# Kernel tuning notes

Measured on AMD Instinct MI355X. Metric: run time of the kernel, lower is better.

The kernel has to match this reference:

```python
import jax, jax.numpy as jnp
import numpy as np

T, K, B, D, ND = 200, 512, 1024, 128, 16
H = D * ND
LOGC = float(np.log(np.sqrt(2.0 * np.pi)))  # log(sqrt(2*pi))


def setup_inputs() -> dict:
    key = jax.random.key(0)
    ks = jax.random.split(key, 16)
    s = 0.02  # xavier-ish init scale
    X = jax.random.normal(ks[0], (T, K, D), jnp.float32)
    M = (jax.random.uniform(ks[1], (T, K, D)) < 0.7).astype(jnp.float32)
    # K unique, sorted sample indices per time step (ragged chunks made uniform)
    batch_idx = jnp.sort(jnp.argsort(jax.random.uniform(ks[2], (T, B)), axis=1)[:, :K], axis=1).astype(jnp.int32)
    obs_times = jnp.arange(1, T + 1, dtype=jnp.float32) * 0.05
    def mat(k, sh):
        return jax.random.normal(k, sh, jnp.float32) * s
    return {
        'obs_times': obs_times, 'X': X, 'M': M,
        'Wp1': mat(ks[3], (H, H)), 'bp1': jnp.zeros((H,), jnp.float32),
        'Wp2': mat(ks[4], (H, 2 * D)), 'bp2': jnp.zeros((2 * D,), jnp.float32),
        'W_r': mat(ks[5], (D, H)), 'V_r': mat(ks[6], (D, H)), 'U_r': mat(ks[7], (H, H)),
        'W_z': mat(ks[8], (D, H)), 'V_z': mat(ks[9], (D, H)), 'U_z': mat(ks[10], (H, H)),
        'W_h': mat(ks[11], (D, H)), 'V_h': mat(ks[12], (D, H)), 'U_h': mat(ks[13], (H, H)),
        'b_r': jnp.zeros((H,), jnp.float32), 'b_z': jnp.zeros((H,), jnp.float32), 'b_h': jnp.zeros((H,), jnp.float32),
        'Wgx': mat(ks[14], (D, D)), 'Wgh': mat(ks[15], (D, H)),
        'batch_idx': batch_idx, 'num_samples': B,
    }


def _forward(obs_times, X, M, Wp1, bp1, Wp2, bp2, W_r, V_r, U_r, W_z, V_z, U_z,
             W_h, V_h, U_h, b_r, b_z, b_h, Wgx, Wgh, batch_idx, num_samples):
    Bn, Dn, Hn = num_samples, W_r.shape[0], W_r.shape[1]
    h0 = jnp.zeros((Bn, Hn), jnp.float32)
    lx0 = jnp.zeros((Bn, Dn), jnp.float32)
    lt0 = jnp.zeros((Bn, Dn), jnp.float32)

    def step(carry, xs):
        h, last_x, last_t, loss, totM = carry
        t, Xo, Mo, idx = xs
        hg = h[idx]  # [K,H] gather of persistent state for observed samples
        # p_model (dropout in eval mode = identity), only observed rows are used
        p = jnp.maximum(hg @ Wp1 + bp1, 0.0) @ Wp2 + bp2  # [K,2D]
        mean, logvar = jnp.split(p, 2, axis=1)
        err = (Xo - mean) * jnp.exp(-0.5 * logvar)
        losses = 0.5 * ((err * err + logvar + 2.0 * LOGC) * Mo)
        # masked last-observation update (scatter)
        lx = last_x[idx] * (1.0 - Mo) + Xo * Mo
        last_x = last_x.at[idx].set(lx)
        mean_x = jnp.sum(Xo, 0, keepdims=True) / jnp.sum(Mo + 1e-6, 0, keepdims=True)
        ltg = last_t[idx]
        iv = t - ltg  # interval uses pre-update last_t (gathered rows only)
        last_t = last_t.at[idx].set(ltg * (1.0 - Mo) + t * Mo)
        gx = jnp.exp(-jnp.maximum(0.0, iv @ Wgx))  # [K,D]
        gh = jnp.exp(-jnp.maximum(0.0, iv @ Wgh))  # [K,H]
        X_hat = Mo * Xo + (1.0 - Mo) * gx * lx + (1.0 - Mo) * (1.0 - gx) * mean_x
        # GRU-D cell on gathered rows, then scatter back
        hd = gh * hg
        r = jax.nn.sigmoid(X_hat @ W_r + hd @ U_r + Mo @ V_r + b_r)
        z = jax.nn.sigmoid(X_hat @ W_z + hd @ U_z + Mo @ V_z + b_z)
        ht = jnp.tanh(X_hat @ W_h + (r * hd) @ U_h + Mo @ V_h + b_h)
        hn = (1.0 - z) * hd + z * ht
        h = h.at[idx].set(hn)
        return (h, last_x, last_t, loss + losses.sum(), totM + Mo.sum()), None

    init = (h0, lx0, lt0, jnp.float32(0.0), jnp.float32(0.0))
    (h, _, _, loss, totM), _ = jax.lax.scan(step, init, (obs_times, X, M, batch_idx))
    return loss / totM


def reference(obs_times, X, M, Wp1, bp1, Wp2, bp2, W_r, V_r, U_r, W_z, V_z, U_z,
              W_h, V_h, U_h, b_r, b_z, b_h, Wgx, Wgh, batch_idx, num_samples):
    return _forward(obs_times, X, M, Wp1, bp1, Wp2, bp2, W_r, V_r, U_r, W_z, V_z,
                    U_z, W_h, V_h, U_h, b_r, b_z, b_h, Wgx, Wgh, batch_idx, num_samples)
```

## Files before the change

kernel.cpp:

```cpp
#include <hip/hip_runtime.h>

#define TT 200
#define KK 512
#define BB 1024
#define DD 128
#define HH 2048

typedef short short8 __attribute__((ext_vector_type(8)));
typedef float f32x4 __attribute__((ext_vector_type(4)));
typedef __bf16 bf16x8 __attribute__((ext_vector_type(8)));

#define TWO_LOGC 1.8378770664093453f

__device__ __forceinline__ unsigned short f2bf(float f) {
  union { float f; unsigned u; } x; x.f = f;
  unsigned r = x.u + 0x7fffu + ((x.u >> 16) & 1u);
  return (unsigned short)(r >> 16);
}
__device__ __forceinline__ float bf2f(unsigned short b) {
  union { unsigned u; float f; } x; x.u = ((unsigned)b) << 16;
  return x.f;
}
__device__ __forceinline__ f32x4 mfma16(short8 a, short8 b, f32x4 c) {
  return __builtin_amdgcn_mfma_f32_16x16x32_bf16(
      __builtin_bit_cast(bf16x8, a), __builtin_bit_cast(bf16x8, b), c, 0, 0, 0);
}

typedef void __attribute__((address_space(1))) as1_void;
typedef void __attribute__((address_space(3))) as3_void;
__device__ __forceinline__ void gld_lds16(const unsigned short* g, unsigned short* l) {
  __builtin_amdgcn_global_load_lds((as1_void*)const_cast<unsigned short*>(g),
                                   (as3_void*)l, 16, 0, 0);
}

struct GP {
  const unsigned short* A1; int lda1;
  const unsigned short* A2; int lda2; int split;
  const unsigned short* BT; int ldb;
  int Kr;
  const float* bias;
  const float* bias2;
  unsigned short* obf;
  unsigned short* obf2;
  float* of1;
  const float* f1;
  const float* f2;
  const float* f3;
  const unsigned short* u1;
  const int* idx;
  float* h;
  float* d_loss;
};

template <int MI, int NI, int EPI>
__global__ __launch_bounds__(256, 2) void gemmP(GP p) {
  constexpr int BM = 32 * MI, BN = 32 * NI;
  constexpr int L = (MI + NI) / 2;
  __shared__ unsigned short As[4][BM * 32];
  __shared__ unsigned short Bs[4][BN * 32];
  const int tid = threadIdx.x;
  const int lane = tid & 63;
  const int w = tid >> 6;
  const int wr = w >> 1, wc = w & 1;
  const long m0 = (long)blockIdx.x * BM;
  const int n0 = blockIdx.y * BN;

  const int lrow = lane >> 2;
  const unsigned short* gA1[L];
  const unsigned short* gA2[L];
  const unsigned short* gB[L];
  unsigned short* lds0[L];
  int sstr[L];
  bool isA[L];
#pragma unroll
  for (int j = 0; j < L; ++j) {
    int c = w * L + j;
    if (c < 2 * MI) {
      int r = c * 16 + lrow;
      int cs = (lane & 3) ^ ((r >> 1) & 3);
      isA[j] = true;
      gA1[j] = p.A1 + (m0 + r) * (long)p.lda1 + cs * 8;
      gA2[j] = p.A2 + (m0 + r) * (long)p.lda2 + cs * 8 - p.split;
      gB[j] = gA1[j];
      lds0[j] = &As[0][c * 512];
      sstr[j] = BM * 32;
    } else {
      int cb = c - 2 * MI;
      int r = cb * 16 + lrow;
      int cs = (lane & 3) ^ ((r >> 1) & 3);
      isA[j] = false;
      gB[j] = p.BT + (long)(n0 + r) * p.ldb + cs * 8;
      gA1[j] = gB[j]; gA2[j] = gB[j];
      lds0[j] = &Bs[0][cb * 512];
      sstr[j] = BN * 32;
    }
  }

  auto stage = [&](int slot, int k0) {
#pragma unroll
    for (int j = 0; j < L; ++j) {
      const unsigned short* g =
          isA[j] ? ((k0 < p.split) ? gA1[j] + k0 : gA2[j] + k0) : gB[j] + k0;
      gld_lds16(g, lds0[j] + slot * sstr[j]);
    }
  };

  const int frow = lane & 15;
  const int fg = lane >> 4;

  f32x4 acc[MI][NI] = {};

  const int nIter = p.Kr >> 5;
  stage(0, 0);
  stage(1, 32);
  stage(2, 64);
  for (int i = 0; i < nIter; ++i) {
    asm volatile("s_waitcnt vmcnt(%0)" ::"i"(2 * L) : "memory");
    __builtin_amdgcn_s_barrier();
    __builtin_amdgcn_sched_barrier(0);
    const int slot = i & 3;
    short8 af[MI], bfr[NI];
#pragma unroll
    for (int mi = 0; mi < MI; ++mi) {
      int r = wr * (16 * MI) + mi * 16 + frow;
      af[mi] = *(const short8*)&As[slot][r * 32 + ((fg ^ ((r >> 1) & 3)) << 3)];
    }
#pragma unroll
    for (int ni = 0; ni < NI; ++ni) {
      int r = wc * (16 * NI) + ni * 16 + frow;
      bfr[ni] = *(const short8*)&Bs[slot][r * 32 + ((fg ^ ((r >> 1) & 3)) << 3)];
    }
#pragma unroll
    for (int mi = 0; mi < MI; ++mi)
#pragma unroll
      for (int ni = 0; ni < NI; ++ni) acc[mi][ni] = mfma16(af[mi], bfr[ni], acc[mi][ni]);
    int j3 = i + 3;
    if (j3 >= nIter) j3 = nIter - 1;
    stage((i + 3) & 3, j3 * 32);
  }

  float lsum = 0.f;
#pragma unroll
  for (int mi = 0; mi < MI; ++mi) {
#pragma unroll
    for (int r = 0; r < 4; ++r) {
      const long grow = m0 + wr * (16 * MI) + mi * 16 + ((lane >> 4) << 2) + r;
      int bi = 0;
      if constexpr (EPI == 2 || EPI == 4) bi = p.idx[grow];
#pragma unroll
      for (int ni = 0; ni < NI; ++ni) {
        const int gcol = n0 + wc * (16 * NI) + ni * 16 + (lane & 15);
        float v = acc[mi][ni][r];
        if constexpr (EPI == 0) {
          v += p.bias[gcol];
          v = fmaxf(v, 0.f);
          p.obf[grow * HH + gcol] = f2bf(v);
        } else if constexpr (EPI == 1) {
          float bsel = (gcol & 1) ? p.bias[128 + (gcol >> 1)] : p.bias[gcol >> 1];
          float vb = v + bsel;
          float pv = __shfl_xor(vb, 1);
          if (!(gcol & 1)) {
            int d = gcol >> 1;
            long o = grow * DD + d;
            float Xo = p.f1[o], Mo = p.f2[o];
            float e = Xo - vb;
            lsum += 0.5f * Mo * (e * e * expf(-pv) + pv + TWO_LOGC);
          }
        } else if constexpr (EPI == 2) {
          float gh = expf(-fmaxf(v, 0.f));
          float hg = p.h[(long)bi * HH + gcol];
          float hd = gh * hg;
          long o = grow * HH + gcol;
          p.obf[o] = f2bf(hg);
          p.obf2[o] = f2bf(hd);
          p.of1[o] = hd;
        } else if constexpr (EPI == 3) {
          if (gcol < HH) {
            float rv = 1.f / (1.f + expf(-(v + p.bias[gcol])));
            long o = grow * HH + gcol;
            p.obf[o] = f2bf(rv * p.f1[o]);
          } else {
            int c = gcol - HH;
            float zv = 1.f / (1.f + expf(-(v + p.bias2[c])));
            p.of1[grow * HH + c] = zv;
          }
        } else if constexpr (EPI == 4) {
          float ht = tanhf(v + p.bias[gcol]);
          long o = grow * HH + gcol;
          float z = p.f1[o], hd = p.f2[o];
          p.h[(long)bi * HH + gcol] = (1.f - z) * hd + z * ht;
        } else {
          int tt = (int)(grow >> 9);
          float gx = expf(-fmaxf(v, 0.f));
          long o = grow * DD + gcol;
          float Xo = p.f1[o], Mo = p.f2[o];
          float lx = bf2f(p.u1[grow * 256 + gcol]);
          float mx = p.f3[(long)tt * DD + gcol];
          float xh = Mo * Xo + (1.f - Mo) * (gx * lx + (1.f - gx) * mx);
          p.obf[grow * 256 + gcol] = f2bf(xh);
        }
      }
    }
  }
  if constexpr (EPI == 1) {
    for (int off = 32; off; off >>= 1) lsum += __shfl_down(lsum, off);
    if (lane == 0) atomicAdd(p.d_loss, lsum);
  }
}

__global__ void transpose_cvt(const float* __restrict__ src, long src_ld,
                              unsigned short* __restrict__ dst, long dst_ld,
                              long row_off, int row_stride, long col_off) {
  __shared__ float tile[32][33];
  int k0 = blockIdx.x * 32, n0 = blockIdx.y * 32;
  int tx = threadIdx.x & 31, ty = threadIdx.x >> 5;
  for (int i = ty; i < 32; i += 8) tile[i][tx] = src[(long)(k0 + i) * src_ld + n0 + tx];
  __syncthreads();
  for (int i = ty; i < 32; i += 8) {
    long n = n0 + i, k = k0 + tx;
    dst[(row_off + n * row_stride) * dst_ld + col_off + k] = f2bf(tile[tx][i]);
  }
}

__global__ void init_k(float* h, float* scal) {
  long i = (long)blockIdx.x * blockDim.x + threadIdx.x;
  if (i < (long)BB * HH) h[i] = 0.f;
  if (i < 2) scal[i] = 0.f;
}
__global__ void pos_init(int* pos) {
  int i = blockIdx.x * 256 + threadIdx.x;
  if (i < TT * BB) pos[i] = -1;
}
__global__ void pos_fill(const int* __restrict__ bidx, int* __restrict__ pos) {
  int i = blockIdx.x * 256 + threadIdx.x;
  if (i < TT * KK) {
    int t = i >> 9, k = i & 511;
    pos[t * BB + bidx[i]] = k;
  }
}
__global__ void traj(const float* __restrict__ X, const float* __restrict__ M,
                     const float* __restrict__ times, const int* __restrict__ pos,
                     unsigned short* __restrict__ iv_bf, unsigned short* __restrict__ XM) {
  int b = blockIdx.x, d = threadIdx.x;
  float lastx = 0.f, lastt = 0.f;
  for (int t = 0; t < TT; ++t) {
    int k = pos[t * BB + b];
    if (k >= 0) {
      long row = (long)t * KK + k;
      long o = row * DD + d;
      float Xo = X[o], Mo = M[o];
      float tv = times[t];
      iv_bf[o] = f2bf(tv - lastt);
      float lx = lastx * (1.f - Mo) + Xo * Mo;
      XM[row * 256 + d] = f2bf(lx);
      lastx = lx;
      lastt = lastt * (1.f - Mo) + tv * Mo;
    }
  }
}
__global__ void meanx_k(const float* __restrict__ X, const float* __restrict__ M,
                        float* __restrict__ mx) {
  int t = blockIdx.x, d = threadIdx.x;
  const float* Xb = X + (long)t * KK * DD;
  const float* Mb = M + (long)t * KK * DD;
  float sx = 0.f, sm = 0.f;
  for (int k = 0; k < KK; ++k) {
    sx += Xb[k * DD + d];
    sm += Mb[k * DD + d];
  }
  mx[t * DD + d] = sx / (sm + KK * 1e-6f);
}
__global__ void totm_k(const float* __restrict__ M, float* __restrict__ scal) {
  long n = (long)TT * KK * DD;
  float v = 0.f;
  for (long i = (long)blockIdx.x * blockDim.x + threadIdx.x; i < n;
       i += (long)gridDim.x * blockDim.x)
    v += M[i];
  for (int off = 32; off; off >>= 1) v += __shfl_down(v, off);
  if ((threadIdx.x & 63) == 0) atomicAdd(&scal[1], v);
}
__global__ void mo_fill(const float* __restrict__ M, unsigned short* __restrict__ XM) {
  long i = (long)blockIdx.x * blockDim.x + threadIdx.x;
  long n = (long)TT * KK * DD;
  if (i < n) {
    long row = i >> 7;
    int d = i & 127;
    XM[row * 256 + 128 + d] = f2bf(M[i]);
  }
}
__global__ void finish_k(const float* scal, float* out) { out[0] = scal[0] / scal[1]; }

extern "C" void kernel_launch(void* const* d_in, const int* in_sizes, int n_in,
                              void* d_out, int out_size, void* d_ws, size_t ws_size,
                              hipStream_t stream) {
  const float* times = (const float*)d_in[0];
  const float* X = (const float*)d_in[1];
  const float* M = (const float*)d_in[2];
  const float* Wp1 = (const float*)d_in[3];
  const float* bp1 = (const float*)d_in[4];
  const float* Wp2 = (const float*)d_in[5];
  const float* bp2 = (const float*)d_in[6];
  const float* W_r = (const float*)d_in[7];
  const float* V_r = (const float*)d_in[8];
  const float* U_r = (const float*)d_in[9];
  const float* W_z = (const float*)d_in[10];
  const float* V_z = (const float*)d_in[11];
  const float* U_z = (const float*)d_in[12];
  const float* W_h = (const float*)d_in[13];
  const float* V_h = (const float*)d_in[14];
  const float* U_h = (const float*)d_in[15];
  const float* b_r = (const float*)d_in[16];
  const float* b_z = (const float*)d_in[17];
  const float* b_h = (const float*)d_in[18];
  const float* Wgx = (const float*)d_in[19];
  const float* Wgh = (const float*)d_in[20];
  const int* bidx = (const int*)d_in[21];

  char* wp = (char*)d_ws;
  auto alloc = [&](size_t n) {
    char* r = wp;
    wp += (n + 1023) & ~(size_t)1023;
    return r;
  };
  float* h = (float*)alloc((size_t)BB * HH * 4);
  unsigned short* P1T = (unsigned short*)alloc((size_t)HH * HH * 2);
  unsigned short* P2T = (unsigned short*)alloc((size_t)256 * HH * 2);
  unsigned short* GxT = (unsigned short*)alloc((size_t)DD * DD * 2);
  unsigned short* GhT = (unsigned short*)alloc((size_t)HH * DD * 2);
  unsigned short* B4T = (unsigned short*)alloc((size_t)2 * HH * 2304 * 2);
  unsigned short* B5T = (unsigned short*)alloc((size_t)HH * 2304 * 2);
  unsigned short* iv_bf = (unsigned short*)alloc((size_t)TT * KK * DD * 2);
  unsigned short* XM = (unsigned short*)alloc((size_t)TT * KK * 256 * 2);
  float* meanx = (float*)alloc((size_t)TT * DD * 4);
  int* pos = (int*)alloc((size_t)TT * BB * 4);
  unsigned short* hd_bf = (unsigned short*)alloc((size_t)KK * HH * 2);
  float* hd_f32 = (float*)alloc((size_t)KK * HH * 4);
  unsigned short* rh_bf = (unsigned short*)alloc((size_t)KK * HH * 2);
  float* zbuf = (float*)alloc((size_t)KK * HH * 4);
  float* scal = (float*)alloc(1024);

  size_t used = (size_t)(wp - (char*)d_ws);
  size_t slot = (size_t)KK * HH * 2;
  long rem = (long)ws_size - (long)used;
  int NB = (int)(rem / (long)(2 * slot));
  if (NB < 1) NB = 1;
  if (NB > 50) NB = 50;
  unsigned short* hgr = (unsigned short*)alloc(slot * NB);
  unsigned short* A1r = (unsigned short*)alloc(slot * NB);

  dim3 blk(256);

  init_k<<<(BB * HH + 255) / 256, blk, 0, stream>>>(h, scal);
  pos_init<<<(TT * BB + 255) / 256, blk, 0, stream>>>(pos);
  pos_fill<<<(TT * KK + 255) / 256, blk, 0, stream>>>(bidx, pos);

  auto tc = [&](const float* src, long src_ld, unsigned short* dst, long dst_ld, int KR,
                int NC, long row_off, int row_stride, long col_off) {
    transpose_cvt<<<dim3(KR / 32, NC / 32), blk, 0, stream>>>(src, src_ld, dst, dst_ld,
                                                              row_off, row_stride, col_off);
  };
  tc(Wp1, HH, P1T, HH, HH, HH, 0, 1, 0);
  tc(Wp2, 256, P2T, HH, HH, 128, 0, 2, 0);
  tc(Wp2 + 128, 256, P2T, HH, HH, 128, 1, 2, 0);
  tc(Wgx, DD, GxT, DD, DD, DD, 0, 1, 0);
  tc(Wgh, HH, GhT, DD, DD, HH, 0, 1, 0);
  tc(U_r, HH, B4T, 2304, HH, HH, 0, 1, 0);
  tc(W_r, HH, B4T, 2304, DD, HH, 0, 1, 2048);
  tc(V_r, HH, B4T, 2304, DD, HH, 0, 1, 2176);
  tc(U_z, HH, B4T, 2304, HH, HH, 2048, 1, 0);
  tc(W_z, HH, B4T, 2304, DD, HH, 2048, 1, 2048);
  tc(V_z, HH, B4T, 2304, DD, HH, 2048, 1, 2176);
  tc(U_h, HH, B5T, 2304, HH, HH, 0, 1, 0);
  tc(W_h, HH, B5T, 2304, DD, HH, 0, 1, 2048);
  tc(V_h, HH, B5T, 2304, DD, HH, 0, 1, 2176);

  meanx_k<<<TT, dim3(DD), 0, stream>>>(X, M, meanx);
  traj<<<BB, dim3(DD), 0, stream>>>(X, M, times, pos, iv_bf, XM);
  totm_k<<<1024, blk, 0, stream>>>(M, scal);
  mo_fill<<<(TT * KK * DD + 255) / 256, blk, 0, stream>>>(M, XM);

  {
    GP g = {};
    g.A1 = iv_bf; g.lda1 = DD; g.A2 = iv_bf; g.lda2 = DD; g.split = 1 << 30;
    g.BT = GxT; g.ldb = DD; g.Kr = DD;
    g.f1 = X; g.f2 = M; g.f3 = meanx; g.u1 = XM; g.obf = XM;
    gemmP<2, 4, 5><<<dim3(TT * KK / 64, 1), blk, 0, stream>>>(g);
  }

  int t0 = 0;
  for (int t = 0; t < TT; ++t) {
    const int* idx_t = bidx + t * KK;
    const unsigned short* XMt = XM + (size_t)t * KK * 256;
    unsigned short* hg_t = hgr + (size_t)(t - t0) * KK * HH;
    {
      GP g = {};
      g.A1 = iv_bf + (size_t)t * KK * DD; g.lda1 = DD;
      g.A2 = g.A1; g.lda2 = DD; g.split = 1 << 30;
      g.BT = GhT; g.ldb = DD; g.Kr = DD;
      g.obf = hg_t; g.obf2 = hd_bf; g.of1 = hd_f32; g.idx = idx_t; g.h = h;
      gemmP<2, 2, 2><<<dim3(KK / 64, HH / 64), blk, 0, stream>>>(g);
    }
    {
      GP g = {};
      g.A1 = hd_bf; g.lda1 = HH; g.A2 = XMt; g.lda2 = 256; g.split = HH;
      g.BT = B4T; g.ldb = 2304; g.Kr = 2304;
      g.bias = b_r; g.bias2 = b_z; g.obf = rh_bf; g.f1 = hd_f32; g.of1 = zbuf;
      gemmP<4, 2, 3><<<dim3(KK / 128, 2 * HH / 64), blk, 0, stream>>>(g);
    }
    {
      GP g = {};
      g.A1 = rh_bf; g.lda1 = HH; g.A2 = XMt; g.lda2 = 256; g.split = HH;
      g.BT = B5T; g.ldb = 2304; g.Kr = 2304;
      g.bias = b_h; g.f1 = zbuf; g.f2 = hd_f32; g.idx = idx_t; g.h = h;
      gemmP<2, 2, 4><<<dim3(KK / 64, HH / 64), blk, 0, stream>>>(g);
    }
    if (t - t0 + 1 == NB || t == TT - 1) {
      int cnt = t - t0 + 1;
      {
        GP g = {};
        g.A1 = hgr; g.lda1 = HH; g.A2 = hgr; g.lda2 = HH; g.split = 1 << 30;
        g.BT = P1T; g.ldb = HH; g.Kr = HH;
        g.bias = bp1; g.obf = A1r;
        gemmP<4, 4, 0><<<dim3(cnt * KK / 128, HH / 128), blk, 0, stream>>>(g);
      }
      {
        GP g = {};
        g.A1 = A1r; g.lda1 = HH; g.A2 = A1r; g.lda2 = HH; g.split = 1 << 30;
        g.BT = P2T; g.ldb = HH; g.Kr = HH;
        g.bias = bp2; g.f1 = X + (size_t)t0 * KK * DD; g.f2 = M + (size_t)t0 * KK * DD;
        g.d_loss = scal;
        gemmP<4, 4, 1><<<dim3(cnt * KK / 128, 256 / 128), blk, 0, stream>>>(g);
      }
      t0 = t + 1;
    }
  }
  finish_k<<<1, 1, 0, stream>>>(scal, (float*)d_out);
}
```

Measured before the change: 14.03 ms.

## Fuse per-step GRU GEMMs into one persistent kernel with grid barriers

Merges the three per-timestep GEMM launches (gate/gather, r/z gates, candidate/update) into a single 256-block kernel that runs the phases back to back, separated by an atomic-counter grid barrier. The hd and z intermediates are now kept in bf16 instead of fp32, which removes the fp32 hd buffer and halves the z traffic. The aim is to cut launch overhead and tail gaps between the small per-step kernels, which repeat 200 times. In exchange, the fused kernel relies on all 256 blocks being resident at once for the spin barrier, and the bf16 intermediates lower precision in the recurrence.

```diff
diff --git a/kernel.cpp b/kernel.cpp
--- a/kernel.cpp
+++ b/kernel.cpp
@@ -47,23 +47,23 @@
   const float* f2;
   const float* f3;
   const unsigned short* u1;
+  const unsigned short* u2;
   const int* idx;
   float* h;
   float* d_loss;
 };
 
-template <int MI, int NI, int EPI>
-__global__ __launch_bounds__(256, 2) void gemmP(GP p) {
+template <int MI, int NI, int EPI, int ASTR, int BSTR>
+__device__ __forceinline__ void gphase(const GP p, unsigned short* AsB,
+                                       unsigned short* BsB, int bx, int by) {
   constexpr int BM = 32 * MI, BN = 32 * NI;
   constexpr int L = (MI + NI) / 2;
-  __shared__ unsigned short As[4][BM * 32];
-  __shared__ unsigned short Bs[4][BN * 32];
   const int tid = threadIdx.x;
   const int lane = tid & 63;
   const int w = tid >> 6;
   const int wr = w >> 1, wc = w & 1;
-  const long m0 = (long)blockIdx.x * BM;
-  const int n0 = blockIdx.y * BN;
+  const long m0 = (long)bx * BM;
+  const int n0 = by * BN;
 
   const int lrow = lane >> 2;
   const unsigned short* gA1[L];
@@ -82,8 +82,8 @@
       gA1[j] = p.A1 + (m0 + r) * (long)p.lda1 + cs * 8;
       gA2[j] = p.A2 + (m0 + r) * (long)p.lda2 + cs * 8 - p.split;
       gB[j] = gA1[j];
-      lds0[j] = &As[0][c * 512];
-      sstr[j] = BM * 32;
+      lds0[j] = AsB + c * 512;
+      sstr[j] = ASTR;
     } else {
       int cb = c - 2 * MI;
       int r = cb * 16 + lrow;
@@ -91,8 +91,8 @@
       isA[j] = false;
       gB[j] = p.BT + (long)(n0 + r) * p.ldb + cs * 8;
       gA1[j] = gB[j]; gA2[j] = gB[j];
-      lds0[j] = &Bs[0][cb * 512];
-      sstr[j] = BN * 32;
+      lds0[j] = BsB + cb * 512;
+      sstr[j] = BSTR;
     }
   }
 
@@ -123,12 +123,12 @@
 #pragma unroll
     for (int mi = 0; mi < MI; ++mi) {
       int r = wr * (16 * MI) + mi * 16 + frow;
-      af[mi] = *(const short8*)&As[slot][r * 32 + ((fg ^ ((r >> 1) & 3)) << 3)];
+      af[mi] = *(const short8*)&AsB[slot * ASTR + r * 32 + ((fg ^ ((r >> 1) & 3)) << 3)];
     }
 #pragma unroll
     for (int ni = 0; ni < NI; ++ni) {
       int r = wc * (16 * NI) + ni * 16 + frow;
-      bfr[ni] = *(const short8*)&Bs[slot][r * 32 + ((fg ^ ((r >> 1) & 3)) << 3)];
+      bfr[ni] = *(const short8*)&BsB[slot * BSTR + r * 32 + ((fg ^ ((r >> 1) & 3)) << 3)];
     }
 #pragma unroll
     for (int mi = 0; mi < MI; ++mi)
@@ -138,6 +138,7 @@
     if (j3 >= nIter) j3 = nIter - 1;
     stage((i + 3) & 3, j3 * 32);
   }
+  asm volatile("s_waitcnt vmcnt(0)" ::: "memory");
 
   float lsum = 0.f;
 #pragma unroll
@@ -173,21 +174,20 @@
           long o = grow * HH + gcol;
           p.obf[o] = f2bf(hg);
           p.obf2[o] = f2bf(hd);
-          p.of1[o] = hd;
         } else if constexpr (EPI == 3) {
           if (gcol < HH) {
             float rv = 1.f / (1.f + expf(-(v + p.bias[gcol])));
             long o = grow * HH + gcol;
-            p.obf[o] = f2bf(rv * p.f1[o]);
+            p.obf[o] = f2bf(rv * bf2f(p.u1[o]));
           } else {
             int c = gcol - HH;
             float zv = 1.f / (1.f + expf(-(v + p.bias2[c])));
-            p.of1[grow * HH + c] = zv;
+            p.obf2[grow * HH + c] = f2bf(zv);
           }
         } else if constexpr (EPI == 4) {
           float ht = tanhf(v + p.bias[gcol]);
           long o = grow * HH + gcol;
-          float z = p.f1[o], hd = p.f2[o];
+          float z = bf2f(p.u1[o]), hd = bf2f(p.u2[o]);
           p.h[(long)bi * HH + gcol] = (1.f - z) * hd + z * ht;
         } else {
           int tt = (int)(grow >> 9);
@@ -208,6 +208,38 @@
   }
 }
 
+template <int MI, int NI, int EPI>
+__global__ __launch_bounds__(256, 2) void gemmP(GP p) {
+  __shared__ unsigned short As[4][32 * MI * 32];
+  __shared__ unsigned short Bs[4][32 * NI * 32];
+  gphase<MI, NI, EPI, 32 * MI * 32, 32 * NI * 32>(p, &As[0][0], &Bs[0][0],
+                                                  blockIdx.x, blockIdx.y);
+}
+
+__device__ __forceinline__ void gbar(unsigned* cnt, unsigned gen) {
+  __syncthreads();
+  if (threadIdx.x == 0) {
+    __threadfence();
+    atomicAdd(cnt, 1u);
+    const unsigned want = gen * 256u;
+    while (atomicAdd(cnt, 0u) < want) __builtin_amdgcn_s_sleep(2);
+    __threadfence();
+  }
+  __syncthreads();
+}
+
+__global__ __launch_bounds__(256, 2) void step_fused(GP s1, GP s4, GP s5,
+                                                     unsigned* gsync, unsigned gen0) {
+  __shared__ unsigned short As[4][4096];
+  __shared__ unsigned short Bs[4][2048];
+  const int bid = blockIdx.x;
+  gphase<2, 2, 2, 4096, 2048>(s1, &As[0][0], &Bs[0][0], bid & 7, bid >> 3);
+  gbar(gsync, gen0 + 1);
+  gphase<4, 2, 3, 4096, 2048>(s4, &As[0][0], &Bs[0][0], bid & 3, bid >> 2);
+  gbar(gsync, gen0 + 2);
+  gphase<2, 2, 4, 4096, 2048>(s5, &As[0][0], &Bs[0][0], bid & 7, bid >> 3);
+}
+
 __global__ void transpose_cvt(const float* __restrict__ src, long src_ld,
                               unsigned short* __restrict__ dst, long dst_ld,
                               long row_off, int row_stride, long col_off) {
@@ -225,7 +257,7 @@
 __global__ void init_k(float* h, float* scal) {
   long i = (long)blockIdx.x * blockDim.x + threadIdx.x;
   if (i < (long)BB * HH) h[i] = 0.f;
-  if (i < 2) scal[i] = 0.f;
+  if (i < 16) scal[i] = 0.f;
 }
 __global__ void pos_init(int* pos) {
   int i = blockIdx.x * 256 + threadIdx.x;
@@ -334,10 +366,10 @@
   float* meanx = (float*)alloc((size_t)TT * DD * 4);
   int* pos = (int*)alloc((size_t)TT * BB * 4);
   unsigned short* hd_bf = (unsigned short*)alloc((size_t)KK * HH * 2);
-  float* hd_f32 = (float*)alloc((size_t)KK * HH * 4);
   unsigned short* rh_bf = (unsigned short*)alloc((size_t)KK * HH * 2);
-  float* zbuf = (float*)alloc((size_t)KK * HH * 4);
+  unsigned short* z_bf = (unsigned short*)alloc((size_t)KK * HH * 2);
   float* scal = (float*)alloc(1024);
+  unsigned* gsync = (unsigned*)(scal + 2);
 
   size_t used = (size_t)(wp - (char*)d_ws);
   size_t slot = (size_t)KK * HH * 2;
@@ -392,28 +424,19 @@
     const int* idx_t = bidx + t * KK;
     const unsigned short* XMt = XM + (size_t)t * KK * 256;
     unsigned short* hg_t = hgr + (size_t)(t - t0) * KK * HH;
-    {
-      GP g = {};
-      g.A1 = iv_bf + (size_t)t * KK * DD; g.lda1 = DD;
-      g.A2 = g.A1; g.lda2 = DD; g.split = 1 << 30;
-      g.BT = GhT; g.ldb = DD; g.Kr = DD;
-      g.obf = hg_t; g.obf2 = hd_bf; g.of1 = hd_f32; g.idx = idx_t; g.h = h;
-      gemmP<2, 2, 2><<<dim3(KK / 64, HH / 64), blk, 0, stream>>>(g);
-    }
-    {
-      GP g = {};
-      g.A1 = hd_bf; g.lda1 = HH; g.A2 = XMt; g.lda2 = 256; g.split = HH;
-      g.BT = B4T; g.ldb = 2304; g.Kr = 2304;
-      g.bias = b_r; g.bias2 = b_z; g.obf = rh_bf; g.f1 = hd_f32; g.of1 = zbuf;
-      gemmP<4, 2, 3><<<dim3(KK / 128, 2 * HH / 64), blk, 0, stream>>>(g);
-    }
-    {
-      GP g = {};
-      g.A1 = rh_bf; g.lda1 = HH; g.A2 = XMt; g.lda2 = 256; g.split = HH;
-      g.BT = B5T; g.ldb = 2304; g.Kr = 2304;
-      g.bias = b_h; g.f1 = zbuf; g.f2 = hd_f32; g.idx = idx_t; g.h = h;
-      gemmP<2, 2, 4><<<dim3(KK / 64, HH / 64), blk, 0, stream>>>(g);
-    }
+    GP g1 = {}, g4 = {}, g5 = {};
+    g1.A1 = iv_bf + (size_t)t * KK * DD; g1.lda1 = DD;
+    g1.A2 = g1.A1; g1.lda2 = DD; g1.split = 1 << 30;
+    g1.BT = GhT; g1.ldb = DD; g1.Kr = DD;
+    g1.obf = hg_t; g1.obf2 = hd_bf; g1.idx = idx_t; g1.h = h;
+    g4.A1 = hd_bf; g4.lda1 = HH; g4.A2 = XMt; g4.lda2 = 256; g4.split = HH;
+    g4.BT = B4T; g4.ldb = 2304; g4.Kr = 2304;
+    g4.bias = b_r; g4.bias2 = b_z; g4.obf = rh_bf; g4.obf2 = z_bf; g4.u1 = hd_bf;
+    g5.A1 = rh_bf; g5.lda1 = HH; g5.A2 = XMt; g5.lda2 = 256; g5.split = HH;
+    g5.BT = B5T; g5.ldb = 2304; g5.Kr = 2304;
+    g5.bias = b_h; g5.u1 = z_bf; g5.u2 = hd_bf; g5.idx = idx_t; g5.h = h;
+    step_fused<<<dim3(256), blk, 0, stream>>>(g1, g4, g5, gsync, 2 * (unsigned)t);
+
     if (t - t0 + 1 == NB || t == TT - 1) {
       int cnt = t - t0 + 1;
       {
```

Result: slower. 20.58 ms (+46.7%).
